# Kernel tuning notes

Measured on AMD Instinct MI355X. Metric: run time of the kernel, lower is better.

## Reference

```python
import jax, jax.numpy as jnp
import numpy as np

N = 50000   # nodes
E = 800000  # directed edges (avg degree 16)
IN, HID, OUT = 128, 128, 64


def setup_inputs() -> dict:
    key = jax.random.key(0)
    k1, k2, k3, k4 = jax.random.split(key, 4)
    x = jax.random.normal(k1, (N, IN), dtype=jnp.float32)
    edge_index = jax.random.randint(k2, (2, E), 0, N, dtype=jnp.int64)
    W1 = jax.random.normal(k3, (IN, HID), dtype=jnp.float32) * (1.0 / np.sqrt(IN))
    b1 = jnp.zeros((HID,), dtype=jnp.float32)
    W2 = jax.random.normal(k4, (HID, OUT), dtype=jnp.float32) * (1.0 / np.sqrt(HID))
    b2 = jnp.zeros((OUT,), dtype=jnp.float32)
    return {"x": x, "edge_index": edge_index, "W1": W1, "b1": b1, "W2": W2, "b2": b2}


def _gcn_conv(x, src, dst, deg_inv_sqrt, W, b):
    # PyG GCNConv: h = X @ W; out_i = sum_j norm_ij * h_j  (edges incl. self-loops); out += b
    h = x @ W                                   # [N, F_out]
    norm = deg_inv_sqrt[src] * deg_inv_sqrt[dst]  # [E+N]
    msg = h[src] * norm[:, None]                # gather + scale
    out = jax.ops.segment_sum(msg, dst, num_segments=x.shape[0])  # scatter-add
    return out + b


def reference(x, edge_index, W1, b1, W2, b2):
    n = x.shape[0]
    loop = jnp.arange(n, dtype=edge_index.dtype)
    # add self-loops once; shared by both layers
    src = jnp.concatenate([edge_index[0], loop])
    dst = jnp.concatenate([edge_index[1], loop])
    deg = jax.ops.segment_sum(jnp.ones_like(src, dtype=x.dtype), dst, num_segments=n)
    deg_inv_sqrt = jnp.where(deg > 0, jax.lax.rsqrt(jnp.maximum(deg, 1.0)), 0.0)

    h = _gcn_conv(x, src, dst, deg_inv_sqrt, W1, b1)
    h = jax.nn.relu(h)
    out = _gcn_conv(h, src, dst, deg_inv_sqrt, W2, b2)
    return out
```

## Files before the change

### kernel.cpp

```cpp
#include <hip/hip_runtime.h>

typedef unsigned short u16;
typedef unsigned int u32;
typedef __attribute__((ext_vector_type(8))) short bf16x8;
typedef __attribute__((ext_vector_type(4))) float f32x4;

#define IN_F 128
#define CAP  8192
#define EPB  2048

__device__ inline float bf2f(u16 v) {
    return __uint_as_float(((unsigned)v) << 16);
}
__device__ inline u16 f2bf(float f) {
    unsigned u = __float_as_uint(f);
    return (u16)((u + 0x7fffu + ((u >> 16) & 1u)) >> 16);
}

__device__ inline int block_scan_excl(int v, int* sdat) {
    int tid = threadIdx.x;
    sdat[tid] = v;
    __syncthreads();
#pragma unroll
    for (int off = 1; off < 256; off <<= 1) {
        int t = (tid >= off) ? sdat[tid - off] : 0;
        __syncthreads();
        sdat[tid] += t;
        __syncthreads();
    }
    return sdat[tid] - v;
}


template<int M>
__device__ inline void packW_body(const float* __restrict__ W, u16* __restrict__ Wp, int t) {
    constexpr int NCT = M / 16;
    int l  = t & 63;
    int q  = t >> 6;
    int kt = q & 3;
    int q2 = q >> 2;
    int ct = q2 % NCT;
    int h  = q2 / NCT;
    int col   = 16 * ct + (l & 15);
    int krow0 = 32 * kt + 8 * (l >> 4);
    u16* outp = Wp + (size_t)t * 8;
#pragma unroll
    for (int r = 0; r < 8; ++r) {
        float w  = W[(size_t)(krow0 + r) * M + col];
        u16 hi   = f2bf(w);
        outp[r] = (h == 0) ? hi : f2bf(w - bf2f(hi));
    }
}

__global__ __launch_bounds__(256) void k_setup(const float* __restrict__ W1,
                                               const float* __restrict__ W2,
                                               u16* __restrict__ w1p,
                                               u16* __restrict__ w2p,
                                               int* bcur, int nbuk) {
    int t = blockIdx.x * 256 + threadIdx.x;
    if (t < nbuk) bcur[t] = 0;
    if (t < 2 * 8 * 4 * 64) packW_body<128>(W1, w1p, t);
    if (t < 2 * 4 * 4 * 64) packW_body<64>(W2, w2p, t);
}


__global__ __launch_bounds__(256) void k_ag1(const float* __restrict__ X,
                                             const u16* __restrict__ Wp,
                                             u16* __restrict__ Y,
                                             const int* __restrict__ ei,
                                             int* bcur, u32* __restrict__ tmp,
                                             int E, int n, int nbuk, int gb) {
    constexpr int NCT = 8;
    constexpr int WPW = 2 * NCT * 4 * 64 * 8;
    __shared__ u16 wlds[WPW];
    __shared__ int hist[256];
    const int tid = threadIdx.x;

    if (blockIdx.x < gb) {
        for (int i = tid; i < WPW / 8; i += 256)
            ((uint4*)wlds)[i] = ((const uint4*)Wp)[i];
        __syncthreads();
        const int wid = tid >> 6;
        const int l   = tid & 63;
        const int lr  = l & 15;
        const int lg  = l >> 4;
#pragma unroll
        for (int rt = 0; rt < 4; ++rt) {
            const int row0 = blockIdx.x * 256 + rt * 64 + wid * 16;
            const int arow = row0 + lr;
            const bool rowok = arow < n;
            const float* xr = X + (size_t)arow * 128;
            bf16x8 ahi[4], alo[4];
#pragma unroll
            for (int kt = 0; kt < 4; ++kt) {
                float v[8];
                if (rowok) {
                    float4 p0 = *(const float4*)(xr + 32 * kt + 8 * lg);
                    float4 p1 = *(const float4*)(xr + 32 * kt + 8 * lg + 4);
                    v[0] = p0.x; v[1] = p0.y; v[2] = p0.z; v[3] = p0.w;
                    v[4] = p1.x; v[5] = p1.y; v[6] = p1.z; v[7] = p1.w;
                } else {
#pragma unroll
                    for (int r = 0; r < 8; ++r) v[r] = 0.f;
                }
#pragma unroll
                for (int r = 0; r < 8; ++r) {
                    u16 hi = f2bf(v[r]);
                    ahi[kt][r] = (short)hi;
                    alo[kt][r] = (short)f2bf(v[r] - bf2f(hi));
                }
            }
#pragma unroll
            for (int ct = 0; ct < NCT; ++ct) {
                f32x4 acc = {0.f, 0.f, 0.f, 0.f};
                const u16* whi = wlds + (size_t)(ct * 4) * 512 + l * 8;
                const u16* wlo = whi + (size_t)NCT * 4 * 512;
#pragma unroll
                for (int kt = 0; kt < 4; ++kt) {
                    bf16x8 bh = *(const bf16x8*)(whi + kt * 512);
                    bf16x8 bl = *(const bf16x8*)(wlo + kt * 512);
                    acc = __builtin_amdgcn_mfma_f32_16x16x32_bf16(ahi[kt], bh, acc, 0, 0, 0);
                    acc = __builtin_amdgcn_mfma_f32_16x16x32_bf16(alo[kt], bh, acc, 0, 0, 0);
                    acc = __builtin_amdgcn_mfma_f32_16x16x32_bf16(ahi[kt], bl, acc, 0, 0, 0);
                }
#pragma unroll
                for (int r = 0; r < 4; ++r) {
                    int row = row0 + lg * 4 + r;
                    if (row < n) Y[(size_t)row * 128 + 16 * ct + lr] = f2bf(acc[r]);
                }
            }
        }
    } else {
        const int b = blockIdx.x - gb;
        const int EN = E + n;
        const int t0 = b * EPB;
        const int t1 = min(t0 + EPB, EN);
        hist[tid] = 0;
        __syncthreads();
        for (int t = t0 + tid * 4; t < t1; t += 1024) {
            if (t + 4 <= t1 && t + 4 <= E) {
                int4 d4 = *(const int4*)(ei + E + t);
                atomicAdd(&hist[d4.x >> 8], 1);
                atomicAdd(&hist[d4.y >> 8], 1);
                atomicAdd(&hist[d4.z >> 8], 1);
                atomicAdd(&hist[d4.w >> 8], 1);
            } else {
#pragma unroll
                for (int j = 0; j < 4; ++j) {
                    int tt = t + j;
                    if (tt >= t1) break;
                    int d = (tt < E) ? ei[E + tt] : (tt - E);
                    atomicAdd(&hist[d >> 8], 1);
                }
            }
        }
        __syncthreads();
        if (tid < nbuk) {
            int r = hist[tid];
            int g = (r > 0) ? atomicAdd(&bcur[tid], r) : 0;
            hist[tid] = tid * CAP + g;
        }
        __syncthreads();
        for (int t = t0 + tid * 4; t < t1; t += 1024) {
            if (t + 4 <= t1 && t + 4 <= E) {
                int4 s4 = *(const int4*)(ei + t);
                int4 d4 = *(const int4*)(ei + E + t);
                int p0 = atomicAdd(&hist[d4.x >> 8], 1);
                int p1 = atomicAdd(&hist[d4.y >> 8], 1);
                int p2 = atomicAdd(&hist[d4.z >> 8], 1);
                int p3 = atomicAdd(&hist[d4.w >> 8], 1);
                if (p0 < ((d4.x >> 8) + 1) * CAP) tmp[p0] = (u32)s4.x | ((u32)(d4.x & 255) << 16);
                if (p1 < ((d4.y >> 8) + 1) * CAP) tmp[p1] = (u32)s4.y | ((u32)(d4.y & 255) << 16);
                if (p2 < ((d4.z >> 8) + 1) * CAP) tmp[p2] = (u32)s4.z | ((u32)(d4.z & 255) << 16);
                if (p3 < ((d4.w >> 8) + 1) * CAP) tmp[p3] = (u32)s4.w | ((u32)(d4.w & 255) << 16);
            } else {
#pragma unroll
                for (int j = 0; j < 4; ++j) {
                    int tt = t + j;
                    if (tt >= t1) break;
                    int s, d;
                    if (tt < E) { s = ei[tt]; d = ei[E + tt]; }
                    else        { s = tt - E; d = s; }
                    int bk = d >> 8;
                    int pos = atomicAdd(&hist[bk], 1);
                    if (pos < (bk + 1) * CAP)
                        tmp[pos] = (u32)s | ((u32)(d & 255) << 16);
                }
            }
        }
    }
}

__global__ __launch_bounds__(256) void k_binB1(const u32* __restrict__ tmp,
                                               const int* __restrict__ bcur,
                                               int* __restrict__ row_ptr,
                                               float* __restrict__ dis,
                                               int n, int nbuk) {
    __shared__ int sdat[256];
    __shared__ int cnt_l[256];
    __shared__ int s_gbase;
    const int b = blockIdx.x;
    const int tid = threadIdx.x;
    int v = (tid < nbuk) ? min(bcur[tid], CAP) : 0;
    int ex0 = block_scan_excl(v, sdat);
    if (tid == b) s_gbase = ex0;
    if (b == nbuk - 1 && tid == 0) row_ptr[n] = sdat[255];
    __syncthreads();
    const int gbase = s_gbase;
    const int total = min(bcur[b], CAP);
    const u32* rec0 = tmp + (size_t)b * CAP;
    cnt_l[tid] = 0;
    __syncthreads();
    for (int i = tid; i < total; i += 256)
        atomicAdd(&cnt_l[rec0[i] >> 16], 1);
    __syncthreads();
    int deg = cnt_l[tid];
    int ex = block_scan_excl(deg, sdat);
    int node = b * 256 + tid;
    if (node < n) {
        row_ptr[node] = gbase + ex;
        dis[node] = rsqrtf((float)deg);
    }
}

__global__ __launch_bounds__(256) void k_binB2(const u32* __restrict__ tmp,
                                               const int* __restrict__ bcur,
                                               const int* __restrict__ row_ptr,
                                               const float* __restrict__ dis,
                                               u32* __restrict__ es, int n) {
    __shared__ int lcur[256];
    __shared__ float ldis[256];
    __shared__ u32 es_lds[CAP];
    const int b = blockIdx.x;
    const int tid = threadIdx.x;
    const int total = min(bcur[b], CAP);
    const int node0 = b * 256;
    const int gbase = row_ptr[node0];
    int node = node0 + tid;
    lcur[tid] = (node < n) ? (row_ptr[node] - gbase) : 0;
    ldis[tid] = (node < n) ? dis[node] : 0.f;
    __syncthreads();
    const u32* rec0 = tmp + (size_t)b * CAP;
    for (int i = tid; i < total; i += 256) {
        u32 rec = rec0[i];
        int dl = rec >> 16;
        int s  = rec & 0xffff;
        float nrm = dis[s] * ldis[dl];
        int p = atomicAdd(&lcur[dl], 1);
        es_lds[p] = (u32)s | ((u32)f2bf(nrm) << 16);
    }
    __syncthreads();
    for (int i = tid; i < total; i += 256)
        es[gbase + i] = es_lds[i];
}


__global__ __launch_bounds__(256) void k_gemm2(const u16* __restrict__ A,
                                               const u16* __restrict__ Wp,
                                               u16* __restrict__ Y, int n) {
    constexpr int NCT = 4;
    constexpr int WPW = 2 * NCT * 4 * 64 * 8;
    __shared__ u16 wlds[WPW];
    for (int i = threadIdx.x; i < WPW / 8; i += 256)
        ((uint4*)wlds)[i] = ((const uint4*)Wp)[i];
    __syncthreads();
    const int wid = threadIdx.x >> 6;
    const int l   = threadIdx.x & 63;
    const int lr  = l & 15;
    const int lg  = l >> 4;
#pragma unroll
    for (int rt = 0; rt < 4; ++rt) {
        const int row0 = blockIdx.x * 256 + rt * 64 + wid * 16;
        const int arow = row0 + lr;
        const bool rowok = arow < n;
        bf16x8 a[4];
#pragma unroll
        for (int kt = 0; kt < 4; ++kt) {
            if (rowok) {
                a[kt] = *(const bf16x8*)(A + (size_t)arow * 128 + 32 * kt + 8 * lg);
            } else {
#pragma unroll
                for (int r = 0; r < 8; ++r) a[kt][r] = 0;
            }
        }
#pragma unroll
        for (int ct = 0; ct < NCT; ++ct) {
            f32x4 acc = {0.f, 0.f, 0.f, 0.f};
            const u16* whi = wlds + (size_t)(ct * 4) * 512 + l * 8;
            const u16* wlo = whi + (size_t)NCT * 4 * 512;
#pragma unroll
            for (int kt = 0; kt < 4; ++kt) {
                bf16x8 bh = *(const bf16x8*)(whi + kt * 512);
                bf16x8 bl = *(const bf16x8*)(wlo + kt * 512);
                acc = __builtin_amdgcn_mfma_f32_16x16x32_bf16(a[kt], bh, acc, 0, 0, 0);
                acc = __builtin_amdgcn_mfma_f32_16x16x32_bf16(a[kt], bl, acc, 0, 0, 0);
            }
#pragma unroll
            for (int r = 0; r < 4; ++r) {
                int row = row0 + lg * 4 + r;
                if (row < n) Y[(size_t)row * 64 + 16 * ct + lr] = f2bf(acc[r]);
            }
        }
    }
}


__global__ __launch_bounds__(256) void k_agg128(const u16* __restrict__ h,
                                                const int* __restrict__ row_ptr,
                                                const u32* __restrict__ es,
                                                const float* __restrict__ bias,
                                                u16* __restrict__ out, int n) {
    int node = blockIdx.x * 8 + (threadIdx.x >> 5);
    if (node >= n) return;
    int l31 = threadIdx.x & 31;
    int beg = row_ptr[node], end = row_ptr[node + 1];
    const u16* hp = h + l31 * 4;
    float a0 = 0.f, a1 = 0.f, a2 = 0.f, a3 = 0.f;
    float b0 = 0.f, b1 = 0.f, b2 = 0.f, b3 = 0.f;
    float c0 = 0.f, c1 = 0.f, c2 = 0.f, c3 = 0.f;
    float d0 = 0.f, d1 = 0.f, d2 = 0.f, d3 = 0.f;
    int e = beg;
    for (; e + 3 < end; e += 4) {
        u32 r0 = es[e], r1 = es[e + 1], r2 = es[e + 2], r3 = es[e + 3];
        ushort4 v0 = *(const ushort4*)(hp + (size_t)(r0 & 0xffff) * 128);
        ushort4 v1 = *(const ushort4*)(hp + (size_t)(r1 & 0xffff) * 128);
        ushort4 v2 = *(const ushort4*)(hp + (size_t)(r2 & 0xffff) * 128);
        ushort4 v3 = *(const ushort4*)(hp + (size_t)(r3 & 0xffff) * 128);
        float w0 = bf2f((u16)(r0 >> 16)), w1 = bf2f((u16)(r1 >> 16));
        float w2 = bf2f((u16)(r2 >> 16)), w3 = bf2f((u16)(r3 >> 16));
        a0 += w0 * bf2f(v0.x); a1 += w0 * bf2f(v0.y);
        a2 += w0 * bf2f(v0.z); a3 += w0 * bf2f(v0.w);
        b0 += w1 * bf2f(v1.x); b1 += w1 * bf2f(v1.y);
        b2 += w1 * bf2f(v1.z); b3 += w1 * bf2f(v1.w);
        c0 += w2 * bf2f(v2.x); c1 += w2 * bf2f(v2.y);
        c2 += w2 * bf2f(v2.z); c3 += w2 * bf2f(v2.w);
        d0 += w3 * bf2f(v3.x); d1 += w3 * bf2f(v3.y);
        d2 += w3 * bf2f(v3.z); d3 += w3 * bf2f(v3.w);
    }
    for (; e < end; ++e) {
        u32 r0 = es[e];
        float w0 = bf2f((u16)(r0 >> 16));
        ushort4 v0 = *(const ushort4*)(hp + (size_t)(r0 & 0xffff) * 128);
        a0 += w0 * bf2f(v0.x); a1 += w0 * bf2f(v0.y);
        a2 += w0 * bf2f(v0.z); a3 += w0 * bf2f(v0.w);
    }
    a0 = (a0 + b0) + (c0 + d0);
    a1 = (a1 + b1) + (c1 + d1);
    a2 = (a2 + b2) + (c2 + d2);
    a3 = (a3 + b3) + (c3 + d3);
    float4 bv = *(const float4*)(bias + 4 * l31);
    a0 = fmaxf(a0 + bv.x, 0.f);
    a1 = fmaxf(a1 + bv.y, 0.f);
    a2 = fmaxf(a2 + bv.z, 0.f);
    a3 = fmaxf(a3 + bv.w, 0.f);
    ushort4 o;
    o.x = f2bf(a0); o.y = f2bf(a1); o.z = f2bf(a2); o.w = f2bf(a3);
    *(ushort4*)(out + (size_t)node * 128 + 4 * l31) = o;
}


__global__ __launch_bounds__(256) void k_agg64(const u16* __restrict__ h,
                                               const int* __restrict__ row_ptr,
                                               const u32* __restrict__ es,
                                               const float* __restrict__ bias,
                                               float* __restrict__ out, int n) {
    int node = blockIdx.x * 16 + (threadIdx.x >> 4);
    if (node >= n) return;
    int l16 = threadIdx.x & 15;
    int beg = row_ptr[node], end = row_ptr[node + 1];
    const u16* hp = h + l16 * 4;
    float a0 = 0.f, a1 = 0.f, a2 = 0.f, a3 = 0.f;
    float b0 = 0.f, b1 = 0.f, b2 = 0.f, b3 = 0.f;
    float c0 = 0.f, c1 = 0.f, c2 = 0.f, c3 = 0.f;
    float d0 = 0.f, d1 = 0.f, d2 = 0.f, d3 = 0.f;
    int e = beg;
    for (; e + 3 < end; e += 4) {
        u32 r0 = es[e], r1 = es[e + 1], r2 = es[e + 2], r3 = es[e + 3];
        ushort4 v0 = *(const ushort4*)(hp + (size_t)(r0 & 0xffff) * 64);
        ushort4 v1 = *(const ushort4*)(hp + (size_t)(r1 & 0xffff) * 64);
        ushort4 v2 = *(const ushort4*)(hp + (size_t)(r2 & 0xffff) * 64);
        ushort4 v3 = *(const ushort4*)(hp + (size_t)(r3 & 0xffff) * 64);
        float w0 = bf2f((u16)(r0 >> 16)), w1 = bf2f((u16)(r1 >> 16));
        float w2 = bf2f((u16)(r2 >> 16)), w3 = bf2f((u16)(r3 >> 16));
        a0 += w0 * bf2f(v0.x); a1 += w0 * bf2f(v0.y);
        a2 += w0 * bf2f(v0.z); a3 += w0 * bf2f(v0.w);
        b0 += w1 * bf2f(v1.x); b1 += w1 * bf2f(v1.y);
        b2 += w1 * bf2f(v1.z); b3 += w1 * bf2f(v1.w);
        c0 += w2 * bf2f(v2.x); c1 += w2 * bf2f(v2.y);
        c2 += w2 * bf2f(v2.z); c3 += w2 * bf2f(v2.w);
        d0 += w3 * bf2f(v3.x); d1 += w3 * bf2f(v3.y);
        d2 += w3 * bf2f(v3.z); d3 += w3 * bf2f(v3.w);
    }
    for (; e < end; ++e) {
        u32 r0 = es[e];
        float w0 = bf2f((u16)(r0 >> 16));
        ushort4 v0 = *(const ushort4*)(hp + (size_t)(r0 & 0xffff) * 64);
        a0 += w0 * bf2f(v0.x); a1 += w0 * bf2f(v0.y);
        a2 += w0 * bf2f(v0.z); a3 += w0 * bf2f(v0.w);
    }
    a0 = (a0 + b0) + (c0 + d0);
    a1 = (a1 + b1) + (c1 + d1);
    a2 = (a2 + b2) + (c2 + d2);
    a3 = (a3 + b3) + (c3 + d3);
    float4 bv = *(const float4*)(bias + 4 * l16);
    float4 o;
    o.x = a0 + bv.x; o.y = a1 + bv.y; o.z = a2 + bv.z; o.w = a3 + bv.w;
    *(float4*)(out + (size_t)node * 64 + 4 * l16) = o;
}


static inline char* alignp(char* p, size_t a) {
    return (char*)(((uintptr_t)p + a - 1) & ~(uintptr_t)(a - 1));
}

extern "C" void kernel_launch(void* const* d_in, const int* in_sizes, int n_in,
                              void* d_out, int out_size, void* d_ws, size_t ws_size,
                              hipStream_t stream) {
    const float* x  = (const float*)d_in[0];
    const int*   ei = (const int*)d_in[1];
    const float* W1 = (const float*)d_in[2];
    const float* b1 = (const float*)d_in[3];
    const float* W2 = (const float*)d_in[4];
    const float* b2 = (const float*)d_in[5];
    float* out = (float*)d_out;

    const int n     = in_sizes[0] / IN_F;
    const int E     = in_sizes[1] / 2;
    const int EN    = E + n;
    const int NBUK  = (n + 255) / 256;
    const int GB    = (n + 255) / 256;
    const int NBLKA = (EN + EPB - 1) / EPB;

    char* w = (char*)d_ws;
    int*   row_ptr  = (int*)w;   w = alignp(w + (size_t)(n + 1) * 4, 256);
    int*   bcur     = (int*)w;   w = alignp(w + (size_t)NBUK * 4, 256);
    float* dis      = (float*)w; w = alignp(w + (size_t)n * 4, 256);
    u32*   tmp      = (u32*)w;   w = alignp(w + (size_t)NBUK * CAP * 4, 256);
    u32*   es       = (u32*)w;   w = alignp(w + (size_t)EN * 4, 256);
    u16*   w1p      = (u16*)w;   w = alignp(w + (size_t)2 * 8 * 4 * 64 * 8 * 2, 256);
    u16*   w2p      = (u16*)w;   w = alignp(w + (size_t)2 * 4 * 4 * 64 * 8 * 2, 256);
    u16*   h1b      = (u16*)w;   w = alignp(w + (size_t)n * 128 * 2, 256);
    u16*   a1b      = (u16*)w;   w = alignp(w + (size_t)n * 128 * 2, 256);
    u16*   h2b      = h1b;

    k_setup<<<16, 256, 0, stream>>>(W1, W2, w1p, w2p, bcur, NBUK);
    k_ag1<<<GB + NBLKA, 256, 0, stream>>>(x, w1p, h1b, ei, bcur, tmp, E, n, NBUK, GB);
    k_binB1<<<NBUK, 256, 0, stream>>>(tmp, bcur, row_ptr, dis, n, NBUK);
    k_binB2<<<NBUK, 256, 0, stream>>>(tmp, bcur, row_ptr, dis, es, n);

    k_agg128<<<(n + 7) / 8, 256, 0, stream>>>(h1b, row_ptr, es, b1, a1b, n);
    k_gemm2<<<GB, 256, 0, stream>>>(a1b, w2p, h2b, n);
    k_agg64<<<(n + 15) / 16, 256, 0, stream>>>(h2b, row_ptr, es, b2, out, n);
}
```

Before: 117.4 us.

## Fuse layer-1 aggregation with layer-2 GEMM via LDS staging

Merges the 128-wide aggregation kernel and the second-layer MFMA GEMM into one kernel. Each block aggregates 16 nodes into an LDS stage tile, then four wavefronts multiply that tile by W2, which is held in LDS, and write the 64-wide h2 directly. This removes the round trip of the intermediate activation through global memory and one kernel launch. In exchange every block reloads W2 (16KB) into LDS and adds a barrier, which may reduce occupancy for the latency-bound gather.

```diff
diff --git a/kernel.cpp b/kernel.cpp
--- a/kernel.cpp
+++ b/kernel.cpp
@@ -255,107 +255,97 @@
 }
 
 
-__global__ __launch_bounds__(256) void k_gemm2(const u16* __restrict__ A,
-                                               const u16* __restrict__ Wp,
-                                               u16* __restrict__ Y, int n) {
-    constexpr int NCT = 4;
-    constexpr int WPW = 2 * NCT * 4 * 64 * 8;
-    __shared__ u16 wlds[WPW];
-    for (int i = threadIdx.x; i < WPW / 8; i += 256)
-        ((uint4*)wlds)[i] = ((const uint4*)Wp)[i];
-    __syncthreads();
-    const int wid = threadIdx.x >> 6;
-    const int l   = threadIdx.x & 63;
-    const int lr  = l & 15;
-    const int lg  = l >> 4;
-#pragma unroll
-    for (int rt = 0; rt < 4; ++rt) {
-        const int row0 = blockIdx.x * 256 + rt * 64 + wid * 16;
-        const int arow = row0 + lr;
-        const bool rowok = arow < n;
-        bf16x8 a[4];
-#pragma unroll
-        for (int kt = 0; kt < 4; ++kt) {
-            if (rowok) {
-                a[kt] = *(const bf16x8*)(A + (size_t)arow * 128 + 32 * kt + 8 * lg);
-            } else {
-#pragma unroll
-                for (int r = 0; r < 8; ++r) a[kt][r] = 0;
-            }
+__global__ __launch_bounds__(256) void k_agg128f(const u16* __restrict__ h,
+                                                 const int* __restrict__ row_ptr,
+                                                 const u32* __restrict__ es,
+                                                 const float* __restrict__ bias,
+                                                 const u16* __restrict__ w2p,
+                                                 u16* __restrict__ h2b, int n) {
+    constexpr int W2W = 2 * 4 * 4 * 64 * 8;
+    __shared__ u16 w2lds[W2W];
+    __shared__ u16 stage[16][136];
+    const int tid = threadIdx.x;
+    for (int i = tid; i < W2W / 8; i += 256)
+        ((uint4*)w2lds)[i] = ((const uint4*)w2p)[i];
+
+    const int hw  = tid >> 5;
+    const int l31 = tid & 31;
+    const u16* hp = h + l31 * 4;
+    const float4 bv = *(const float4*)(bias + 4 * l31);
+
+#pragma unroll
+    for (int round = 0; round < 2; ++round) {
+        const int nodeLocal = round * 8 + hw;
+        const int node = blockIdx.x * 16 + nodeLocal;
+        float a0 = 0.f, a1 = 0.f, a2 = 0.f, a3 = 0.f;
+        if (node < n) {
+            int beg = row_ptr[node], end = row_ptr[node + 1];
+            float b0 = 0.f, b1_ = 0.f, b2_ = 0.f, b3_ = 0.f;
+            float c0 = 0.f, c1 = 0.f, c2 = 0.f, c3 = 0.f;
+            float d0 = 0.f, d1 = 0.f, d2 = 0.f, d3 = 0.f;
+            int e = beg;
+            for (; e + 3 < end; e += 4) {
+                u32 r0 = es[e], r1 = es[e + 1], r2 = es[e + 2], r3 = es[e + 3];
+                ushort4 v0 = *(const ushort4*)(hp + (size_t)(r0 & 0xffff) * 128);
+                ushort4 v1 = *(const ushort4*)(hp + (size_t)(r1 & 0xffff) * 128);
+                ushort4 v2 = *(const ushort4*)(hp + (size_t)(r2 & 0xffff) * 128);
+                ushort4 v3 = *(const ushort4*)(hp + (size_t)(r3 & 0xffff) * 128);
+                float w0 = bf2f((u16)(r0 >> 16)), w1 = bf2f((u16)(r1 >> 16));
+                float w2 = bf2f((u16)(r2 >> 16)), w3 = bf2f((u16)(r3 >> 16));
+                a0 += w0 * bf2f(v0.x); a1 += w0 * bf2f(v0.y);
+                a2 += w0 * bf2f(v0.z); a3 += w0 * bf2f(v0.w);
+                b0 += w1 * bf2f(v1.x); b1_ += w1 * bf2f(v1.y);
+                b2_ += w1 * bf2f(v1.z); b3_ += w1 * bf2f(v1.w);
+                c0 += w2 * bf2f(v2.x); c1 += w2 * bf2f(v2.y);
+                c2 += w2 * bf2f(v2.z); c3 += w2 * bf2f(v2.w);
+                d0 += w3 * bf2f(v3.x); d1 += w3 * bf2f(v3.y);
+                d2 += w3 * bf2f(v3.z); d3 += w3 * bf2f(v3.w);
+            }
+            for (; e < end; ++e) {
+                u32 r0 = es[e];
+                float w0 = bf2f((u16)(r0 >> 16));
+                ushort4 v0 = *(const ushort4*)(hp + (size_t)(r0 & 0xffff) * 128);
+                a0 += w0 * bf2f(v0.x); a1 += w0 * bf2f(v0.y);
+                a2 += w0 * bf2f(v0.z); a3 += w0 * bf2f(v0.w);
+            }
+            a0 = (a0 + b0) + (c0 + d0);
+            a1 = (a1 + b1_) + (c1 + d1);
+            a2 = (a2 + b2_) + (c2 + d2);
+            a3 = (a3 + b3_) + (c3 + d3);
+            a0 = fmaxf(a0 + bv.x, 0.f);
+            a1 = fmaxf(a1 + bv.y, 0.f);
+            a2 = fmaxf(a2 + bv.z, 0.f);
+            a3 = fmaxf(a3 + bv.w, 0.f);
         }
-#pragma unroll
-        for (int ct = 0; ct < NCT; ++ct) {
-            f32x4 acc = {0.f, 0.f, 0.f, 0.f};
-            const u16* whi = wlds + (size_t)(ct * 4) * 512 + l * 8;
-            const u16* wlo = whi + (size_t)NCT * 4 * 512;
-#pragma unroll
-            for (int kt = 0; kt < 4; ++kt) {
-                bf16x8 bh = *(const bf16x8*)(whi + kt * 512);
-                bf16x8 bl = *(const bf16x8*)(wlo + kt * 512);
-                acc = __builtin_amdgcn_mfma_f32_16x16x32_bf16(a[kt], bh, acc, 0, 0, 0);
-                acc = __builtin_amdgcn_mfma_f32_16x16x32_bf16(a[kt], bl, acc, 0, 0, 0);
-            }
-#pragma unroll
-            for (int r = 0; r < 4; ++r) {
-                int row = row0 + lg * 4 + r;
-                if (row < n) Y[(size_t)row * 64 + 16 * ct + lr] = f2bf(acc[r]);
-            }
-        }
-    }
-}
-
-
-__global__ __launch_bounds__(256) void k_agg128(const u16* __restrict__ h,
-                                                const int* __restrict__ row_ptr,
-                                                const u32* __restrict__ es,
-                                                const float* __restrict__ bias,
-                                                u16* __restrict__ out, int n) {
-    int node = blockIdx.x * 8 + (threadIdx.x >> 5);
-    if (node >= n) return;
-    int l31 = threadIdx.x & 31;
-    int beg = row_ptr[node], end = row_ptr[node + 1];
-    const u16* hp = h + l31 * 4;
-    float a0 = 0.f, a1 = 0.f, a2 = 0.f, a3 = 0.f;
-    float b0 = 0.f, b1 = 0.f, b2 = 0.f, b3 = 0.f;
-    float c0 = 0.f, c1 = 0.f, c2 = 0.f, c3 = 0.f;
-    float d0 = 0.f, d1 = 0.f, d2 = 0.f, d3 = 0.f;
-    int e = beg;
-    for (; e + 3 < end; e += 4) {
-        u32 r0 = es[e], r1 = es[e + 1], r2 = es[e + 2], r3 = es[e + 3];
-        ushort4 v0 = *(const ushort4*)(hp + (size_t)(r0 & 0xffff) * 128);
-        ushort4 v1 = *(const ushort4*)(hp + (size_t)(r1 & 0xffff) * 128);
-        ushort4 v2 = *(const ushort4*)(hp + (size_t)(r2 & 0xffff) * 128);
-        ushort4 v3 = *(const ushort4*)(hp + (size_t)(r3 & 0xffff) * 128);
-        float w0 = bf2f((u16)(r0 >> 16)), w1 = bf2f((u16)(r1 >> 16));
-        float w2 = bf2f((u16)(r2 >> 16)), w3 = bf2f((u16)(r3 >> 16));
-        a0 += w0 * bf2f(v0.x); a1 += w0 * bf2f(v0.y);
-        a2 += w0 * bf2f(v0.z); a3 += w0 * bf2f(v0.w);
-        b0 += w1 * bf2f(v1.x); b1 += w1 * bf2f(v1.y);
-        b2 += w1 * bf2f(v1.z); b3 += w1 * bf2f(v1.w);
-        c0 += w2 * bf2f(v2.x); c1 += w2 * bf2f(v2.y);
-        c2 += w2 * bf2f(v2.z); c3 += w2 * bf2f(v2.w);
-        d0 += w3 * bf2f(v3.x); d1 += w3 * bf2f(v3.y);
-        d2 += w3 * bf2f(v3.z); d3 += w3 * bf2f(v3.w);
-    }
-    for (; e < end; ++e) {
-        u32 r0 = es[e];
-        float w0 = bf2f((u16)(r0 >> 16));
-        ushort4 v0 = *(const ushort4*)(hp + (size_t)(r0 & 0xffff) * 128);
-        a0 += w0 * bf2f(v0.x); a1 += w0 * bf2f(v0.y);
-        a2 += w0 * bf2f(v0.z); a3 += w0 * bf2f(v0.w);
-    }
-    a0 = (a0 + b0) + (c0 + d0);
-    a1 = (a1 + b1) + (c1 + d1);
-    a2 = (a2 + b2) + (c2 + d2);
-    a3 = (a3 + b3) + (c3 + d3);
-    float4 bv = *(const float4*)(bias + 4 * l31);
-    a0 = fmaxf(a0 + bv.x, 0.f);
-    a1 = fmaxf(a1 + bv.y, 0.f);
-    a2 = fmaxf(a2 + bv.z, 0.f);
-    a3 = fmaxf(a3 + bv.w, 0.f);
-    ushort4 o;
-    o.x = f2bf(a0); o.y = f2bf(a1); o.z = f2bf(a2); o.w = f2bf(a3);
-    *(ushort4*)(out + (size_t)node * 128 + 4 * l31) = o;
+        ushort4 o;
+        o.x = f2bf(a0); o.y = f2bf(a1); o.z = f2bf(a2); o.w = f2bf(a3);
+        *(ushort4*)(&stage[nodeLocal][4 * l31]) = o;
+    }
+    __syncthreads();
+
+    const int ct = tid >> 6;
+    const int l  = tid & 63;
+    const int lr = l & 15;
+    const int lg = l >> 4;
+    bf16x8 a[4];
+#pragma unroll
+    for (int kt = 0; kt < 4; ++kt)
+        a[kt] = *(const bf16x8*)(&stage[lr][32 * kt + 8 * lg]);
+    f32x4 acc = {0.f, 0.f, 0.f, 0.f};
+    const u16* whi = w2lds + (size_t)(ct * 4) * 512 + l * 8;
+    const u16* wlo = whi + (size_t)4 * 4 * 512;
+#pragma unroll
+    for (int kt = 0; kt < 4; ++kt) {
+        bf16x8 bh = *(const bf16x8*)(whi + kt * 512);
+        bf16x8 bl = *(const bf16x8*)(wlo + kt * 512);
+        acc = __builtin_amdgcn_mfma_f32_16x16x32_bf16(a[kt], bh, acc, 0, 0, 0);
+        acc = __builtin_amdgcn_mfma_f32_16x16x32_bf16(a[kt], bl, acc, 0, 0, 0);
+    }
+#pragma unroll
+    for (int r = 0; r < 4; ++r) {
+        int row = blockIdx.x * 16 + lg * 4 + r;
+        if (row < n) h2b[(size_t)row * 64 + 16 * ct + lr] = f2bf(acc[r]);
+    }
 }
 
 
@@ -440,15 +430,13 @@
     u16*   w1p      = (u16*)w;   w = alignp(w + (size_t)2 * 8 * 4 * 64 * 8 * 2, 256);
     u16*   w2p      = (u16*)w;   w = alignp(w + (size_t)2 * 4 * 4 * 64 * 8 * 2, 256);
     u16*   h1b      = (u16*)w;   w = alignp(w + (size_t)n * 128 * 2, 256);
-    u16*   a1b      = (u16*)w;   w = alignp(w + (size_t)n * 128 * 2, 256);
-    u16*   h2b      = h1b;
+    u16*   h2b      = (u16*)w;   w = alignp(w + (size_t)n * 64 * 2, 256);
 
     k_setup<<<16, 256, 0, stream>>>(W1, W2, w1p, w2p, bcur, NBUK);
     k_ag1<<<GB + NBLKA, 256, 0, stream>>>(x, w1p, h1b, ei, bcur, tmp, E, n, NBUK, GB);
     k_binB1<<<NBUK, 256, 0, stream>>>(tmp, bcur, row_ptr, dis, n, NBUK);
     k_binB2<<<NBUK, 256, 0, stream>>>(tmp, bcur, row_ptr, dis, es, n);
 
-    k_agg128<<<(n + 7) / 8, 256, 0, stream>>>(h1b, row_ptr, es, b1, a1b, n);
-    k_gemm2<<<GB, 256, 0, stream>>>(a1b, w2p, h2b, n);
+    k_agg128f<<<(n + 15) / 16, 256, 0, stream>>>(h1b, row_ptr, es, b1, w2p, h2b, n);
     k_agg64<<<(n + 15) / 16, 256, 0, stream>>>(h2b, row_ptr, es, b2, out, n);
 }
```

Measured after the change: 126.7 us. 7.9% more time.
